# Kernel optimization log

Measured on AMD Instinct MI355X. Metric: run time of the kernel, lower is better.

Reference implementation:

```python
import jax, jax.numpy as jnp
import numpy as np

B, S, D = 8, 1024, 1024
H = 16
DK = D // H  # 64, dim_k == dim_v
F = 4096
EPS = 1e-5


def _layernorm(x, w, b):
    mu = jnp.mean(x, axis=-1, keepdims=True)
    var = jnp.mean((x - mu) ** 2, axis=-1, keepdims=True)
    return (x - mu) * jax.lax.rsqrt(var + EPS) * w + b


def setup_inputs() -> dict:
    key = jax.random.key(0)
    ks = jax.random.split(key, 12)
    init = lambda k, shape: (jax.random.normal(k, shape, dtype=jnp.float32) * 0.02)
    return {
        "src": jax.random.normal(ks[0], (B, S, D), dtype=jnp.float32),
        "mask": jnp.zeros((S, S), dtype=jnp.float32),
        # per-head projections, stacked over heads: [H, D, DK]
        "Wq": init(ks[1], (H, D, DK)), "bq": jnp.zeros((H, DK), jnp.float32),
        "Wk": init(ks[2], (H, D, DK)), "bk": jnp.zeros((H, DK), jnp.float32),
        "Wv": init(ks[3], (H, D, DK)), "bv": jnp.zeros((H, DK), jnp.float32),
        "Wo": init(ks[4], (H * DK, D)), "bo": jnp.zeros((D,), jnp.float32),
        "ln1_w": jnp.ones((D,), jnp.float32), "ln1_b": jnp.zeros((D,), jnp.float32),
        "W1": init(ks[5], (D, F)), "b1": jnp.zeros((F,), jnp.float32),
        "W2": init(ks[6], (F, D)), "b2": jnp.zeros((D,), jnp.float32),
        "ln2_w": jnp.ones((D,), jnp.float32), "ln2_b": jnp.zeros((D,), jnp.float32),
    }


def reference(src, mask, Wq, bq, Wk, bk, Wv, bv, Wo, bo,
              ln1_w, ln1_b, W1, b1, W2, b2, ln2_w, ln2_b):
    # per-head projections (vectorized over heads): [B, H, S, DK]
    q = jnp.einsum('bsd,hdk->bhsk', src, Wq) + bq[None, :, None, :]
    k = jnp.einsum('bsd,hdk->bhsk', src, Wk) + bk[None, :, None, :]
    v = jnp.einsum('bsd,hdk->bhsk', src, Wv) + bv[None, :, None, :]
    scale = float(DK) ** 0.5
    logits = jnp.einsum('bhsk,bhtk->bhst', q, k) / scale  # [B,H,S,S]
    logits = logits + mask * (-1e9)
    attn = jax.nn.softmax(logits, axis=-1)
    ctx = jnp.einsum('bhst,bhtv->bhsv', attn, v)  # [B,H,S,DK]
    # concat heads along feature dim (head-major order matches torch cat)
    ctx = jnp.transpose(ctx, (0, 2, 1, 3)).reshape(B, S, H * DK)
    attn_out = ctx @ Wo + bo
    x = _layernorm(src + attn_out, ln1_w, ln1_b)
    ffn = jax.nn.relu(x @ W1 + b1) @ W2 + b2
    return _layernorm(x + ffn, ln2_w, ln2_b)
```

## Files before the change

### kernel.cpp

```cpp
#include <hip/hip_runtime.h>

#define BB 8
#define SS 1024
#define DD 1024
#define HH 16
#define DK 64
#define FF 4096
#define MM (BB*SS)

typedef __attribute__((ext_vector_type(8))) short short8;
typedef __attribute__((ext_vector_type(4))) short short4v;
typedef __attribute__((ext_vector_type(4))) float floatx4;

__device__ inline short f2bf(float f) {
  union { float f; unsigned u; } v; v.f = f;
  unsigned r = (v.u + 0x7FFFu + ((v.u >> 16) & 1u)) >> 16;
  return (short)r;
}
__device__ inline float bf2f(unsigned short u) {
  union { unsigned u; float f; } v; v.u = ((unsigned)u) << 16;
  return v.f;
}

__device__ inline void gload_lds16(const void* g, void* l) {
  __builtin_amdgcn_global_load_lds(
      (const __attribute__((address_space(1))) void*)g,
      (__attribute__((address_space(3))) void*)l, 16, 0, 0);
}

__device__ void tr64(const float* __restrict__ s, unsigned short* __restrict__ d,
                     int R, int C, int r0, int c0, float (*ld)[68], int tid) {
  {
    int r = tid >> 2, c16 = (tid & 3) * 16;
#pragma unroll
    for (int i = 0; i < 4; ++i)
      *(float4*)(&ld[r][c16 + i * 4]) =
          *(const float4*)(s + (size_t)(r0 + r) * C + c0 + c16 + i * 4);
  }
  __syncthreads();
  int c = tid >> 2, r16 = (tid & 3) * 16;
  short8 o0, o1;
#pragma unroll
  for (int i = 0; i < 8; ++i) {
    o0[i] = f2bf(ld[r16 + i][c]);
    o1[i] = f2bf(ld[r16 + 8 + i][c]);
  }
  unsigned short* dp = d + (size_t)(c0 + c) * R + r0 + r16;
  *(short8*)(dp) = o0;
  *(short8*)(dp + 8) = o1;
}

__global__ __launch_bounds__(256) void prep_all(
    const float* __restrict__ src,
    const float* __restrict__ Wq, const float* __restrict__ Wk,
    const float* __restrict__ Wv,
    const float* __restrict__ bq, const float* __restrict__ bk,
    const float* __restrict__ bv, const float* __restrict__ Wo,
    unsigned short* __restrict__ srcb, unsigned short* __restrict__ wqkvT,
    float* __restrict__ bqkv, unsigned short* __restrict__ woT) {
  __shared__ float ld[64][68];
  const int bid = blockIdx.x, tid = threadIdx.x;
  if (bid < 4096) {
    int i8 = (bid * 256 + tid) * 8;
    float4 a = *(const float4*)(src + i8);
    float4 b = *(const float4*)(src + i8 + 4);
    short8 o;
    o[0] = f2bf(a.x); o[1] = f2bf(a.y); o[2] = f2bf(a.z); o[3] = f2bf(a.w);
    o[4] = f2bf(b.x); o[5] = f2bf(b.y); o[6] = f2bf(b.z); o[7] = f2bf(b.w);
    *(short8*)(srcb + i8) = o;
  } else if (bid < 4864) {
    int idx = bid - 4096;
    int d0 = (idx & 15) * 64, h = (idx >> 4) & 15, z = idx >> 8;
    const float* W = (z == 0 ? Wq : z == 1 ? Wk : Wv) + (size_t)h * DD * DK;
    {
      int r = tid >> 2, c16 = (tid & 3) * 16;
#pragma unroll
      for (int i = 0; i < 4; ++i)
        *(float4*)(&ld[r][c16 + i * 4]) =
            *(const float4*)(W + (size_t)(d0 + r) * DK + c16 + i * 4);
    }
    __syncthreads();
    int dv = tid >> 2, d16 = (tid & 3) * 16;
    short8 o0, o1;
#pragma unroll
    for (int i = 0; i < 8; ++i) {
      o0[i] = f2bf(ld[d16 + i][dv]);
      o1[i] = f2bf(ld[d16 + 8 + i][dv]);
    }
    unsigned short* dst = wqkvT + (size_t)(z * 1024 + h * 64 + dv) * DD + d0 + d16;
    *(short8*)(dst) = o0;
    *(short8*)(dst + 8) = o1;
  } else if (bid < 4876) {
    int n = (bid - 4864) * 256 + tid;
    int z = n >> 10;
    const float* s = (z == 0 ? bq : z == 1 ? bk : bv);
    bqkv[n] = s[n & 1023];
  } else {
    int idx = bid - 4876;
    tr64(Wo, woT, 1024, 1024, (idx & 15) * 64, (idx >> 4) * 64, ld, tid);
  }
}

__global__ __launch_bounds__(256) void prep2(
    const unsigned short* __restrict__ qkv, const float* __restrict__ mask,
    const float* __restrict__ W1, const float* __restrict__ W2,
    unsigned short* __restrict__ kbb, unsigned short* __restrict__ vtb,
    unsigned short* __restrict__ maskb, unsigned short* __restrict__ w1T,
    unsigned short* __restrict__ w2T) {
  __shared__ float ldf[64][68];
  const int bid = blockIdx.x, tid = threadIdx.x;
  if (bid < 2048) {
    const int t0 = (bid & 15) * 64, h = (bid >> 4) & 15, b = bid >> 8;
    int row = tid >> 2, c = (tid & 3) * 16;
    const unsigned short* s = qkv + (size_t)(b * SS + t0 + row) * 3072 + 1024 + h * 64 + c;
    unsigned short* d = kbb + ((size_t)((b * HH + h) * SS + t0 + row)) * 64 + c;
    *(short8*)(d) = *(const short8*)(s);
    *(short8*)(d + 8) = *(const short8*)(s + 8);
  } else if (bid < 4096) {
    __shared__ unsigned short ld[64][72];
    const int i = bid - 2048;
    const int t0 = (i & 15) * 64, h = (i >> 4) & 15, b = i >> 8;
    {
      int r = tid >> 2, c16 = (tid & 3) * 16;
      const unsigned short* s = qkv + (size_t)(b * SS + t0 + r) * 3072 + 2048 + h * 64 + c16;
      *(short8*)(&ld[r][c16]) = *(const short8*)(s);
      *(short8*)(&ld[r][c16 + 8]) = *(const short8*)(s + 8);
    }
    __syncthreads();
    int dv = tid >> 2, t16 = (tid & 3) * 16;
    short8 o0, o1;
#pragma unroll
    for (int j = 0; j < 8; ++j) {
      o0[j] = (short)ld[t16 + j][dv];
      o1[j] = (short)ld[t16 + 8 + j][dv];
    }
    unsigned short* d = vtb + ((size_t)(b * HH + h) * DK + dv) * SS + t0 + t16;
    *(short8*)(d) = o0;
    *(short8*)(d + 8) = o1;
  } else if (bid < 4608) {
    int i8 = ((bid - 4096) * 256 + tid) * 8;
    float4 a = *(const float4*)(mask + i8);
    float4 b = *(const float4*)(mask + i8 + 4);
    short8 o;
    o[0] = f2bf(a.x * -1e9f); o[1] = f2bf(a.y * -1e9f);
    o[2] = f2bf(a.z * -1e9f); o[3] = f2bf(a.w * -1e9f);
    o[4] = f2bf(b.x * -1e9f); o[5] = f2bf(b.y * -1e9f);
    o[6] = f2bf(b.z * -1e9f); o[7] = f2bf(b.w * -1e9f);
    *(short8*)(maskb + i8) = o;
  } else if (bid < 5632) {
    int i = bid - 4608;
    tr64(W1, w1T, 1024, 4096, (i & 15) * 64, (i >> 4) * 64, ldf, tid);
  } else {
    int i = bid - 5632;
    tr64(W2, w2T, 4096, 1024, (i & 63) * 64, (i >> 6) * 64, ldf, tid);
  }
}

#define BARE __builtin_amdgcn_s_barrier()
#define VM6  asm volatile("s_waitcnt vmcnt(6)" ::: "memory")
#define VM4  asm volatile("s_waitcnt vmcnt(4)" ::: "memory")
#define VM0  asm volatile("s_waitcnt vmcnt(0)" ::: "memory")
#define PH_HINT asm volatile("s_waitcnt lgkmcnt(8)" ::: "memory")
#define PH_SYNC { \
  __builtin_amdgcn_s_barrier(); \
  asm volatile("s_waitcnt lgkmcnt(0)" ::: "memory"); \
  __builtin_amdgcn_sched_barrier(0); }

#define LOAD_A(lA_, mh_) { \
  _Pragma("unroll") for (int m_ = 0; m_ < 4; ++m_) { \
    const int row_ = wr * 128 + (mh_) * 64 + m_ * 16 + lm; \
    _Pragma("unroll") for (int ks_ = 0; ks_ < 2; ++ks_) \
      a[m_][ks_] = *(const short8*)((lA_) + (size_t)row_ * 64 + \
                     (size_t)(((ks_ * 4 + quad) ^ (lm & 7)) * 8)); \
  } }

#define LOAD_B(lB_, nh_) { \
  _Pragma("unroll") for (int n_ = 0; n_ < 2; ++n_) { \
    const int row_ = wc * 64 + (nh_) * 32 + n_ * 16 + lm; \
    _Pragma("unroll") for (int ks_ = 0; ks_ < 2; ++ks_) \
      bfr[nh_][n_][ks_] = *(const short8*)((lB_) + 16384 + (size_t)row_ * 64 + \
                     (size_t)(((ks_ * 4 + quad) ^ (lm & 7)) * 8)); \
  } }

#define STAGE_A(kt_, mh_, lb_) { \
  _Pragma("unroll") for (int c_ = 0; c_ < 2; ++c_) { \
    const int row_ = c_ * 128 + (mh_) * 64; \
    gload_lds16(gA + (size_t)(kt_) * 64 + (size_t)row_ * K, \
                (lb_) + (size_t)(row_ + wave * 8) * 64); \
  } }

#define STAGE_B(kt_, nh_, lb_) { \
  _Pragma("unroll") for (int c_ = 0; c_ < 2; ++c_) { \
    const int row_ = c_ * 128 + hi128 + (nh_) * 32; \
    gload_lds16(gB + (size_t)(kt_) * 64 + (size_t)row_ * K, \
                (lb_) + 16384 + (size_t)(row_ + (wave & 3) * 8) * 64); \
  } }

#define MFMA_PH(mh_, nh_) { \
  __builtin_amdgcn_s_setprio(1); \
  _Pragma("unroll") for (int m_ = 0; m_ < 4; ++m_) \
    _Pragma("unroll") for (int n_ = 0; n_ < 2; ++n_) { \
      acc[(mh_) * 4 + m_][(nh_) * 2 + n_] = __builtin_amdgcn_mfma_f32_16x16x32_bf16( \
          bfr[nh_][n_][0], a[m_][0], acc[(mh_) * 4 + m_][(nh_) * 2 + n_], 0, 0, 0); \
      acc[(mh_) * 4 + m_][(nh_) * 2 + n_] = __builtin_amdgcn_mfma_f32_16x16x32_bf16( \
          bfr[nh_][n_][1], a[m_][1], acc[(mh_) * 4 + m_][(nh_) * 2 + n_], 0, 0, 0); \
    } \
  __builtin_amdgcn_s_setprio(0); }

#define KITER(e_, ST_) { \
  LOAD_A(buf0, 0); LOAD_B(buf0, 0); \
  STAGE_B((e_) + 1, 1, buf1); \
  PH_HINT; PH_SYNC; MFMA_PH(0, 0); BARE; \
  LOAD_B(buf0, 1); \
  if (ST_) STAGE_A((e_) + 2, 0, buf0); \
  PH_SYNC; MFMA_PH(0, 1); BARE; \
  LOAD_A(buf0, 1); \
  if (ST_) STAGE_B((e_) + 2, 0, buf0); \
  PH_SYNC; MFMA_PH(1, 0); BARE; \
  if (ST_) STAGE_A((e_) + 2, 1, buf0); \
  PH_SYNC; MFMA_PH(1, 1); \
  if (ST_) { VM6; } else { VM0; } \
  BARE; \
  LOAD_A(buf1, 0); LOAD_B(buf1, 0); \
  if (ST_) STAGE_B((e_) + 2, 1, buf0); \
  PH_HINT; PH_SYNC; MFMA_PH(0, 0); BARE; \
  LOAD_B(buf1, 1); \
  if (ST_) STAGE_A((e_) + 3, 0, buf1); \
  PH_SYNC; MFMA_PH(0, 1); BARE; \
  LOAD_A(buf1, 1); \
  if (ST_) STAGE_B((e_) + 3, 0, buf1); \
  PH_SYNC; MFMA_PH(1, 0); BARE; \
  if (ST_) { \
    STAGE_A((e_) + 3, 1, buf1); \
    PH_SYNC; MFMA_PH(1, 1); VM6; BARE; \
  } else { \
    PH_SYNC; MFMA_PH(1, 1); \
  } }

template <int RELU>
__global__ __launch_bounds__(512, 2) void gemm256(
    const unsigned short* __restrict__ A, const unsigned short* __restrict__ Bt,
    const float* __restrict__ bias, unsigned short* __restrict__ C,
    int M, int N, int K) {
  extern __shared__ unsigned short lds[];
  unsigned short* buf0 = lds;
  unsigned short* buf1 = lds + 32768;
  const int tid = threadIdx.x;
  const int wave = tid >> 6, lane = tid & 63;
  const int lm = lane & 15, quad = lane >> 4;
  const int wr = wave >> 2, wc = wave & 3;

  const int nwg = gridDim.x;
  const int cpx = nwg >> 3;
  const int id = (blockIdx.x & 7) * cpx + (blockIdx.x >> 3);
  const int nbx = N >> 8;
  const int bx = id % nbx, by = id / nbx;
  const int n0 = bx << 8, m0 = by << 8;

  const int NT = K >> 6;

  const int srow = tid >> 3;
  const int chs = (tid & 7) ^ (srow & 7);
  const int hi128 = (tid >= 256) ? 64 : 0;
  const int r32 = (tid >> 3) & 31;
  const unsigned short* gA = A + (size_t)(m0 + srow) * K + chs * 8;
  const unsigned short* gB = Bt + (size_t)(n0 + r32) * K + chs * 8;

  floatx4 acc[8][4] = {};
  short8 a[4][2], bfr[2][2][2];

  STAGE_A(0, 0, buf0); STAGE_B(0, 0, buf0);
  STAGE_A(0, 1, buf0); STAGE_B(0, 1, buf0);
  STAGE_A(1, 0, buf1); STAGE_B(1, 0, buf1);
  STAGE_A(1, 1, buf1);
  VM6;
  BARE;

  const int TT = NT >> 1;
  for (int i = 0; i < TT - 1; ++i) {
    KITER(2 * i, 1);
  }
  KITER(NT - 2, 0);

#pragma unroll
  for (int mi = 0; mi < 8; ++mi) {
    const int row = m0 + wr * 128 + mi * 16 + lm;
#pragma unroll
    for (int nj = 0; nj < 4; ++nj) {
      const int col = n0 + wc * 64 + nj * 16 + (quad << 2);
      const float4 bv = *(const float4*)(bias + col);
      float vv[4] = {acc[mi][nj][0] + bv.x, acc[mi][nj][1] + bv.y,
                     acc[mi][nj][2] + bv.z, acc[mi][nj][3] + bv.w};
      short4v o;
#pragma unroll
      for (int r = 0; r < 4; ++r) {
        float v = vv[r];
        if (RELU) v = fmaxf(v, 0.f);
        o[r] = f2bf(v);
      }
      *(short4v*)(C + (size_t)row * N + col) = o;
    }
  }
}

#define LOAD_A1(lb_, mh_) { \
  _Pragma("unroll") for (int m_ = 0; m_ < 2; ++m_) { \
    const int row_ = wr * 64 + (mh_) * 32 + m_ * 16 + lm; \
    _Pragma("unroll") for (int ks_ = 0; ks_ < 2; ++ks_) \
      a[m_][ks_] = *(const short8*)((lb_) + (size_t)row_ * 64 + \
                     (size_t)(((ks_ * 4 + quad) ^ (lm & 7)) * 8)); \
  } }

#define LOAD_B1(lb_, nh_) { \
  _Pragma("unroll") for (int n_ = 0; n_ < 2; ++n_) { \
    const int row_ = wc * 64 + (nh_) * 32 + n_ * 16 + lm; \
    _Pragma("unroll") for (int ks_ = 0; ks_ < 2; ++ks_) \
      bfr[nh_][n_][ks_] = *(const short8*)((lb_) + 8192 + (size_t)row_ * 64 + \
                     (size_t)(((ks_ * 4 + quad) ^ (lm & 7)) * 8)); \
  } }

#define STAGE_A1(kt_, mh_, lb_) { \
  gload_lds16(gA + (size_t)(kt_) * 64 + (size_t)((mh_) * 32) * K, \
              (lb_) + (size_t)((mh_) * 32 + hi128 + (wave & 3) * 8) * 64); }

#define STAGE_B1(kt_, nh_, lb_) { \
  _Pragma("unroll") for (int c_ = 0; c_ < 2; ++c_) { \
    const int row_ = c_ * 128 + hi128 + (nh_) * 32; \
    gload_lds16(gB + (size_t)(kt_) * 64 + (size_t)row_ * K, \
                (lb_) + 8192 + (size_t)(row_ + (wave & 3) * 8) * 64); \
  } }

#define MFMA_PH1(mh_, nh_) { \
  __builtin_amdgcn_s_setprio(1); \
  _Pragma("unroll") for (int m_ = 0; m_ < 2; ++m_) \
    _Pragma("unroll") for (int n_ = 0; n_ < 2; ++n_) { \
      acc[(mh_) * 2 + m_][(nh_) * 2 + n_] = __builtin_amdgcn_mfma_f32_16x16x32_bf16( \
          bfr[nh_][n_][0], a[m_][0], acc[(mh_) * 2 + m_][(nh_) * 2 + n_], 0, 0, 0); \
      acc[(mh_) * 2 + m_][(nh_) * 2 + n_] = __builtin_amdgcn_mfma_f32_16x16x32_bf16( \
          bfr[nh_][n_][1], a[m_][1], acc[(mh_) * 2 + m_][(nh_) * 2 + n_], 0, 0, 0); \
    } \
  __builtin_amdgcn_s_setprio(0); }

#define KITER1(e_, ST_) { \
  LOAD_A1(buf0, 0); LOAD_B1(buf0, 0); \
  STAGE_B1((e_) + 1, 1, buf1); \
  PH_SYNC; MFMA_PH1(0, 0); BARE; \
  LOAD_B1(buf0, 1); \
  if (ST_) STAGE_A1((e_) + 2, 0, buf0); \
  PH_SYNC; MFMA_PH1(0, 1); BARE; \
  LOAD_A1(buf0, 1); \
  if (ST_) STAGE_B1((e_) + 2, 0, buf0); \
  PH_SYNC; MFMA_PH1(1, 0); BARE; \
  if (ST_) STAGE_A1((e_) + 2, 1, buf0); \
  PH_SYNC; MFMA_PH1(1, 1); \
  if (ST_) { VM4; } else { VM0; } \
  BARE; \
  LOAD_A1(buf1, 0); LOAD_B1(buf1, 0); \
  if (ST_) STAGE_B1((e_) + 2, 1, buf0); \
  PH_SYNC; MFMA_PH1(0, 0); BARE; \
  LOAD_B1(buf1, 1); \
  if (ST_) STAGE_A1((e_) + 3, 0, buf1); \
  PH_SYNC; MFMA_PH1(0, 1); BARE; \
  LOAD_A1(buf1, 1); \
  if (ST_) STAGE_B1((e_) + 3, 0, buf1); \
  PH_SYNC; MFMA_PH1(1, 0); BARE; \
  if (ST_) { \
    STAGE_A1((e_) + 3, 1, buf1); \
    PH_SYNC; MFMA_PH1(1, 1); VM4; BARE; \
  } else { \
    PH_SYNC; MFMA_PH1(1, 1); \
  } }

__global__ __launch_bounds__(512, 2) void gemm128(
    const unsigned short* __restrict__ A, const unsigned short* __restrict__ Bt,
    const float* __restrict__ bias, unsigned short* __restrict__ C,
    int M, int N, int K) {
  extern __shared__ unsigned short lds[];
  unsigned short* buf0 = lds;
  unsigned short* buf1 = lds + 24576;
  const int tid = threadIdx.x;
  const int wave = tid >> 6, lane = tid & 63;
  const int lm = lane & 15, quad = lane >> 4;
  const int wr = wave >> 2, wc = wave & 3;

  const int nwg = gridDim.x;
  const int cpx = nwg >> 3;
  const int id = (blockIdx.x & 7) * cpx + (blockIdx.x >> 3);
  const int nbx = N >> 8;
  const int bx = id % nbx, by = id / nbx;
  const int n0 = bx << 8, m0 = by << 7;

  const int NT = K >> 6;

  const int srow = tid >> 3;
  const int chs = (tid & 7) ^ (srow & 7);
  const int hi128 = (tid >= 256) ? 64 : 0;
  const int r32 = (tid >> 3) & 31;
  const unsigned short* gA = A + (size_t)(m0 + hi128 + r32) * K + chs * 8;
  const unsigned short* gB = Bt + (size_t)(n0 + r32) * K + chs * 8;

  floatx4 acc[4][4] = {};
  short8 a[2][2], bfr[2][2][2];

  STAGE_A1(0, 0, buf0); STAGE_B1(0, 0, buf0);
  STAGE_A1(0, 1, buf0); STAGE_B1(0, 1, buf0);
  STAGE_A1(1, 0, buf1); STAGE_B1(1, 0, buf1);
  STAGE_A1(1, 1, buf1);
  VM4;
  BARE;

  const int TT = NT >> 1;
  for (int i = 0; i < TT - 1; ++i) {
    KITER1(2 * i, 1);
  }
  KITER1(NT - 2, 0);

#pragma unroll
  for (int mi = 0; mi < 4; ++mi) {
    const int row = m0 + wr * 64 + mi * 16 + lm;
#pragma unroll
    for (int nj = 0; nj < 4; ++nj) {
      const int col = n0 + wc * 64 + nj * 16 + (quad << 2);
      const float4 bv = *(const float4*)(bias + col);
      short4v o;
      o[0] = f2bf(acc[mi][nj][0] + bv.x);
      o[1] = f2bf(acc[mi][nj][1] + bv.y);
      o[2] = f2bf(acc[mi][nj][2] + bv.z);
      o[3] = f2bf(acc[mi][nj][3] + bv.w);
      *(short4v*)(C + (size_t)row * N + col) = o;
    }
  }
}

__global__ __launch_bounds__(512) void attention_flash(
    const unsigned short* __restrict__ qkv, const unsigned short* __restrict__ kb,
    const unsigned short* __restrict__ vt, const unsigned short* __restrict__ maskb,
    unsigned short* __restrict__ ctx) {
  const int flat = blockIdx.x;
  const int bh = (flat & 7) + 8 * (flat >> 6);
  const int qt = (flat >> 3) & 7;
  const int b = bh >> 4, h = bh & 15;
  const int s0 = qt * 128;
  const int tid = threadIdx.x;
  const int wave = tid >> 6, lane = tid & 63;
  const int lm = lane & 15, quad = lane >> 4;

  __shared__ __align__(16) unsigned short Ks[64 * 64];
  __shared__ __align__(16) unsigned short Vs[64 * 64];
  __shared__ __align__(16) unsigned short Ms[128 * 64];
  __shared__ __align__(16) unsigned short Ps[8][16 * 72];

  const unsigned short* qp = qkv + (size_t)(b * SS + s0 + wave * 16 + lm) * 3072 + h * 64;
  const short8 qa0 = *(const short8*)(qp + quad * 8);
  const short8 qa1 = *(const short8*)(qp + quad * 8 + 32);

  const unsigned short* kbase = kb + (size_t)bh * SS * DK;
  const unsigned short* vbase = vt + (size_t)bh * DK * SS;
  const unsigned short* mbase = maskb + (size_t)s0 * SS;

  const int sr = lane >> 3, sj = lane & 7;
  float m_run = -3e38f, l_run = 0.f;
  floatx4 O[4] = {};

  for (int it = 0; it < 16; ++it) {
    const int t0 = it * 64;
    __syncthreads();
    {
      int r = wave * 8 + sr;
      gload_lds16(kbase + (size_t)(t0 + r) * 64 + (size_t)(sj ^ (r & 7)) * 8,
                  (char*)Ks + wave * 1024);
      gload_lds16(vbase + (size_t)r * SS + t0 + (size_t)(sj ^ (r & 7)) * 8,
                  (char*)Vs + wave * 1024);
      int q1 = wave * 8 + sr;
      gload_lds16(mbase + (size_t)q1 * SS + t0 + (size_t)(sj ^ (q1 & 7)) * 8,
                  (char*)Ms + wave * 1024);
      int q2 = 64 + wave * 8 + sr;
      gload_lds16(mbase + (size_t)q2 * SS + t0 + (size_t)(sj ^ (q2 & 7)) * 8,
                  (char*)Ms + 8192 + wave * 1024);
    }
    __syncthreads();

    float p[16];
    float mt = -3e38f;
    const int qr = wave * 16 + lm;
#pragma unroll
    for (int ts = 0; ts < 4; ++ts) {
      int r = ts * 16 + lm;
      short8 kf0 = *(const short8*)&Ks[(r * 8 + (quad ^ (r & 7))) * 8];
      short8 kf1 = *(const short8*)&Ks[(r * 8 + ((quad + 4) ^ (r & 7))) * 8];
      floatx4 c = {0.f, 0.f, 0.f, 0.f};
      c = __builtin_amdgcn_mfma_f32_16x16x32_bf16(kf0, qa0, c, 0, 0, 0);
      c = __builtin_amdgcn_mfma_f32_16x16x32_bf16(kf1, qa1, c, 0, 0, 0);
      int mj = (ts * 2 + (quad >> 1)) ^ (qr & 7);
      short4v mv = *(const short4v*)&Ms[(qr * 8 + mj) * 8 + (quad & 1) * 4];
#pragma unroll
      for (int r2 = 0; r2 < 4; ++r2) {
        float sv = c[r2] * 0.125f + bf2f((unsigned short)mv[r2]);
        p[ts * 4 + r2] = sv;
        mt = fmaxf(mt, sv);
      }
    }
    mt = fmaxf(mt, __shfl_xor(mt, 16));
    mt = fmaxf(mt, __shfl_xor(mt, 32));
    if (!__all(mt - m_run <= 8.f)) {
      float mnew = fmaxf(m_run, mt);
      float alpha = __expf(m_run - mnew);
#pragma unroll
      for (int d = 0; d < 4; ++d)
#pragma unroll
        for (int r2 = 0; r2 < 4; ++r2) O[d][r2] *= alpha;
      l_run *= alpha;
      m_run = mnew;
    }
    float psum = 0.f;
#pragma unroll
    for (int i = 0; i < 16; ++i) { p[i] = __expf(p[i] - m_run); psum += p[i]; }
    psum += __shfl_xor(psum, 16);
    psum += __shfl_xor(psum, 32);
    l_run += psum;

    unsigned short* pw = &Ps[wave][lm * 72];
#pragma unroll
    for (int ts = 0; ts < 4; ++ts) {
      unsigned plo, phi;
      asm("v_cvt_pk_bf16_f32 %0, %1, %2" : "=v"(plo) : "v"(p[ts * 4 + 0]), "v"(p[ts * 4 + 1]));
      asm("v_cvt_pk_bf16_f32 %0, %1, %2" : "=v"(phi) : "v"(p[ts * 4 + 2]), "v"(p[ts * 4 + 3]));
      uint2 pu; pu.x = plo; pu.y = phi;
      *(uint2*)(pw + ts * 16 + quad * 4) = pu;
    }

#pragma unroll
    for (int ks = 0; ks < 2; ++ks) {
      short8 pf = *(const short8*)(pw + ks * 32 + quad * 8);
#pragma unroll
      for (int d = 0; d < 4; ++d) {
        int dv = d * 16 + lm;
        short8 vf = *(const short8*)&Vs[(dv * 8 + ((ks * 4 + quad) ^ (dv & 7))) * 8];
        O[d] = __builtin_amdgcn_mfma_f32_16x16x32_bf16(vf, pf, O[d], 0, 0, 0);
      }
    }
  }

  const float inv = 1.f / l_run;
  unsigned short* cp = ctx + (size_t)(b * SS + s0 + wave * 16 + lm) * DD + h * 64;
#pragma unroll
  for (int d = 0; d < 4; ++d) {
    short4v o;
#pragma unroll
    for (int r2 = 0; r2 < 4; ++r2) o[r2] = f2bf(O[d][r2] * inv);
    *(short4v*)(cp + d * 16 + quad * 4) = o;
  }
}

template <int A_BF16, int OUT_BF16>
__global__ __launch_bounds__(256) void residual_ln(
    const void* __restrict__ a_, const unsigned short* __restrict__ rr,
    const float* __restrict__ w, const float* __restrict__ bias,
    void* __restrict__ out_) {
  const int row = blockIdx.x;
  const int t = threadIdx.x;
  float x[4];
  if (A_BF16) {
    short4v va = *(const short4v*)((const unsigned short*)a_ + (size_t)row * DD + t * 4);
#pragma unroll
    for (int i = 0; i < 4; ++i) x[i] = bf2f((unsigned short)va[i]);
  } else {
    float4 va = *(const float4*)((const float*)a_ + (size_t)row * DD + t * 4);
    x[0] = va.x; x[1] = va.y; x[2] = va.z; x[3] = va.w;
  }
  {
    short4v vr = *(const short4v*)(rr + (size_t)row * DD + t * 4);
#pragma unroll
    for (int i = 0; i < 4; ++i) x[i] += bf2f((unsigned short)vr[i]);
  }
  float s = 0.f, ss = 0.f;
#pragma unroll
  for (int i = 0; i < 4; ++i) { s += x[i]; ss += x[i] * x[i]; }
#pragma unroll
  for (int o = 32; o > 0; o >>= 1) {
    s  += __shfl_down(s, o);
    ss += __shfl_down(ss, o);
  }
  __shared__ float2 sred[4];
  int wid = t >> 6;
  if ((t & 63) == 0) sred[wid] = make_float2(s, ss);
  __syncthreads();
  float st = 0.f, sst = 0.f;
#pragma unroll
  for (int i = 0; i < 4; ++i) { st += sred[i].x; sst += sred[i].y; }
  float mu  = st * (1.f / 1024.f);
  float var = sst * (1.f / 1024.f) - mu * mu;
  float rsq = rsqrtf(var + 1e-5f);
  float4 vw = *(const float4*)(w + t * 4);
  float4 vb = *(const float4*)(bias + t * 4);
  float o[4];
  o[0] = (x[0] - mu) * rsq * vw.x + vb.x;
  o[1] = (x[1] - mu) * rsq * vw.y + vb.y;
  o[2] = (x[2] - mu) * rsq * vw.z + vb.z;
  o[3] = (x[3] - mu) * rsq * vw.w + vb.w;
  if (OUT_BF16) {
    short4v ov;
#pragma unroll
    for (int i = 0; i < 4; ++i) ov[i] = f2bf(o[i]);
    *(short4v*)((unsigned short*)out_ + (size_t)row * DD + t * 4) = ov;
  } else {
    float4 ov = {o[0], o[1], o[2], o[3]};
    *(float4*)((float*)out_ + (size_t)row * DD + t * 4) = ov;
  }
}

extern "C" void kernel_launch(void* const* d_in, const int* in_sizes, int n_in,
                              void* d_out, int out_size, void* d_ws, size_t ws_size,
                              hipStream_t stream) {
  const float* src  = (const float*)d_in[0];
  const float* mask = (const float*)d_in[1];
  const float* Wq = (const float*)d_in[2];  const float* bq = (const float*)d_in[3];
  const float* Wk = (const float*)d_in[4];  const float* bk = (const float*)d_in[5];
  const float* Wv = (const float*)d_in[6];  const float* bv = (const float*)d_in[7];
  const float* Wo = (const float*)d_in[8];  const float* bo = (const float*)d_in[9];
  const float* ln1w = (const float*)d_in[10]; const float* ln1b = (const float*)d_in[11];
  const float* W1 = (const float*)d_in[12]; const float* b1 = (const float*)d_in[13];
  const float* W2 = (const float*)d_in[14]; const float* b2 = (const float*)d_in[15];
  const float* ln2w = (const float*)d_in[16]; const float* ln2b = (const float*)d_in[17];
  float* out = (float*)d_out;

  const size_t NEED = 125841408;
  if (ws_size < NEED) return;

  char* ws = (char*)d_ws;
  unsigned short* qkv   = (unsigned short*)(ws);
  unsigned short* vtb   = (unsigned short*)(ws + 50331648);
  unsigned short* kbb   = (unsigned short*)(ws + 67108864);
  unsigned short* ctxb  = (unsigned short*)(ws + 83886080);
  unsigned short* srcb  = (unsigned short*)(ws + 100663296);
  unsigned short* w1T   = (unsigned short*)(ws + 100663296);
  unsigned short* w2T   = (unsigned short*)(ws + 109051904);
  unsigned short* wqkvT = (unsigned short*)(ws + 117440512);
  unsigned short* maskb = (unsigned short*)(ws + 117440512);
  unsigned short* woT   = (unsigned short*)(ws + 123731968);
  float*          bqkv  = (float*)(ws + 125829120);
  unsigned short* h1       = qkv;
  unsigned short* attn_out = kbb;
  unsigned short* xb       = ctxb;
  unsigned short* ffn      = kbb;

  static bool lds_init = false;
  if (!lds_init) {
    auto* k0 = gemm256<0>;
    auto* k1 = gemm256<1>;
    hipFuncSetAttribute((const void*)k0, hipFuncAttributeMaxDynamicSharedMemorySize, 131072);
    hipFuncSetAttribute((const void*)k1, hipFuncAttributeMaxDynamicSharedMemorySize, 131072);
    hipFuncSetAttribute((const void*)gemm128, hipFuncAttributeMaxDynamicSharedMemorySize, 98304);
    lds_init = true;
  }

  prep_all<<<5132, 256, 0, stream>>>(src, Wq, Wk, Wv, bq, bk, bv, Wo,
                                     srcb, wqkvT, bqkv, woT);
  gemm128<<<(3072 / 256) * (MM / 128), 512, 98304, stream>>>(srcb, wqkvT, bqkv, qkv, MM, 3072, DD);
  prep2<<<6656, 256, 0, stream>>>(qkv, mask, W1, W2, kbb, vtb, maskb, w1T, w2T);
  attention_flash<<<1024, 512, 0, stream>>>(qkv, kbb, vtb, maskb, ctxb);
  gemm128<<<(DD / 256) * (MM / 128), 512, 98304, stream>>>(ctxb, woT, bo, attn_out, MM, DD, DD);
  residual_ln<0, 1><<<MM, 256, 0, stream>>>(src, attn_out, ln1w, ln1b, xb);
  gemm256<1><<<(FF / 256) * (MM / 256), 512, 131072, stream>>>(xb, w1T, b1, h1, MM, FF, DD);
  gemm128<<<(DD / 256) * (MM / 128), 512, 98304, stream>>>(h1, w2T, b2, ffn, MM, DD, FF);
  residual_ln<1, 0><<<MM, 256, 0, stream>>>(xb, ffn, ln2w, ln2b, out);
}
```

Before: 509.8 us.

## Read K directly from QKV buffer and use exp2 softmax in attention

Drops the separate K repack pass in prep2, so attention loads K tiles straight from the strided QKV projection output. The softmax is rewritten in base 2: scale and mask are pre-multiplied by log2(e) so the native exp2 instruction replaces __expf, and the rescale threshold is adjusted to match. The row max is computed with a tree of fmax instead of a serial chain. Strided K reads (3072-element row stride) may coalesce less well than the contiguous repacked layout.

```diff
diff --git a/kernel.cpp b/kernel.cpp
--- a/kernel.cpp
+++ b/kernel.cpp
@@ -104,21 +104,13 @@
 __global__ __launch_bounds__(256) void prep2(
     const unsigned short* __restrict__ qkv, const float* __restrict__ mask,
     const float* __restrict__ W1, const float* __restrict__ W2,
-    unsigned short* __restrict__ kbb, unsigned short* __restrict__ vtb,
-    unsigned short* __restrict__ maskb, unsigned short* __restrict__ w1T,
-    unsigned short* __restrict__ w2T) {
+    unsigned short* __restrict__ vtb, unsigned short* __restrict__ maskb,
+    unsigned short* __restrict__ w1T, unsigned short* __restrict__ w2T) {
   __shared__ float ldf[64][68];
   const int bid = blockIdx.x, tid = threadIdx.x;
   if (bid < 2048) {
-    const int t0 = (bid & 15) * 64, h = (bid >> 4) & 15, b = bid >> 8;
-    int row = tid >> 2, c = (tid & 3) * 16;
-    const unsigned short* s = qkv + (size_t)(b * SS + t0 + row) * 3072 + 1024 + h * 64 + c;
-    unsigned short* d = kbb + ((size_t)((b * HH + h) * SS + t0 + row)) * 64 + c;
-    *(short8*)(d) = *(const short8*)(s);
-    *(short8*)(d + 8) = *(const short8*)(s + 8);
-  } else if (bid < 4096) {
     __shared__ unsigned short ld[64][72];
-    const int i = bid - 2048;
+    const int i = bid;
     const int t0 = (i & 15) * 64, h = (i >> 4) & 15, b = i >> 8;
     {
       int r = tid >> 2, c16 = (tid & 3) * 16;
@@ -137,21 +129,22 @@
     unsigned short* d = vtb + ((size_t)(b * HH + h) * DK + dv) * SS + t0 + t16;
     *(short8*)(d) = o0;
     *(short8*)(d + 8) = o1;
-  } else if (bid < 4608) {
-    int i8 = ((bid - 4096) * 256 + tid) * 8;
+  } else if (bid < 2560) {
+    const float MS = -1.442695041e9f;
+    int i8 = ((bid - 2048) * 256 + tid) * 8;
     float4 a = *(const float4*)(mask + i8);
     float4 b = *(const float4*)(mask + i8 + 4);
     short8 o;
-    o[0] = f2bf(a.x * -1e9f); o[1] = f2bf(a.y * -1e9f);
-    o[2] = f2bf(a.z * -1e9f); o[3] = f2bf(a.w * -1e9f);
-    o[4] = f2bf(b.x * -1e9f); o[5] = f2bf(b.y * -1e9f);
-    o[6] = f2bf(b.z * -1e9f); o[7] = f2bf(b.w * -1e9f);
+    o[0] = f2bf(a.x * MS); o[1] = f2bf(a.y * MS);
+    o[2] = f2bf(a.z * MS); o[3] = f2bf(a.w * MS);
+    o[4] = f2bf(b.x * MS); o[5] = f2bf(b.y * MS);
+    o[6] = f2bf(b.z * MS); o[7] = f2bf(b.w * MS);
     *(short8*)(maskb + i8) = o;
-  } else if (bid < 5632) {
-    int i = bid - 4608;
+  } else if (bid < 3584) {
+    int i = bid - 2560;
     tr64(W1, w1T, 1024, 4096, (i & 15) * 64, (i >> 4) * 64, ldf, tid);
   } else {
-    int i = bid - 5632;
+    int i = bid - 3584;
     tr64(W2, w2T, 4096, 1024, (i & 63) * 64, (i >> 6) * 64, ldf, tid);
   }
 }
@@ -433,9 +426,8 @@
 }
 
 __global__ __launch_bounds__(512) void attention_flash(
-    const unsigned short* __restrict__ qkv, const unsigned short* __restrict__ kb,
-    const unsigned short* __restrict__ vt, const unsigned short* __restrict__ maskb,
-    unsigned short* __restrict__ ctx) {
+    const unsigned short* __restrict__ qkv, const unsigned short* __restrict__ vt,
+    const unsigned short* __restrict__ maskb, unsigned short* __restrict__ ctx) {
   const int flat = blockIdx.x;
   const int bh = (flat & 7) + 8 * (flat >> 6);
   const int qt = (flat >> 3) & 7;
@@ -454,11 +446,13 @@
   const short8 qa0 = *(const short8*)(qp + quad * 8);
   const short8 qa1 = *(const short8*)(qp + quad * 8 + 32);
 
-  const unsigned short* kbase = kb + (size_t)bh * SS * DK;
+  const unsigned short* kbase = qkv + (size_t)b * SS * 3072 + 1024 + h * 64;
   const unsigned short* vbase = vt + (size_t)bh * DK * SS;
   const unsigned short* mbase = maskb + (size_t)s0 * SS;
 
   const int sr = lane >> 3, sj = lane & 7;
+  const int srr = wave * 8 + sr;
+  const unsigned short* ksrc = kbase + (size_t)srr * 3072 + (size_t)(sj ^ (srr & 7)) * 8;
   float m_run = -3e38f, l_run = 0.f;
   floatx4 O[4] = {};
 
@@ -466,10 +460,8 @@
     const int t0 = it * 64;
     __syncthreads();
     {
-      int r = wave * 8 + sr;
-      gload_lds16(kbase + (size_t)(t0 + r) * 64 + (size_t)(sj ^ (r & 7)) * 8,
-                  (char*)Ks + wave * 1024);
-      gload_lds16(vbase + (size_t)r * SS + t0 + (size_t)(sj ^ (r & 7)) * 8,
+      gload_lds16(ksrc + (size_t)t0 * 3072, (char*)Ks + wave * 1024);
+      gload_lds16(vbase + (size_t)srr * SS + t0 + (size_t)(sj ^ (srr & 7)) * 8,
                   (char*)Vs + wave * 1024);
       int q1 = wave * 8 + sr;
       gload_lds16(mbase + (size_t)q1 * SS + t0 + (size_t)(sj ^ (q1 & 7)) * 8,
@@ -481,7 +473,6 @@
     __syncthreads();
 
     float p[16];
-    float mt = -3e38f;
     const int qr = wave * 16 + lm;
 #pragma unroll
     for (int ts = 0; ts < 4; ++ts) {
@@ -495,16 +486,20 @@
       short4v mv = *(const short4v*)&Ms[(qr * 8 + mj) * 8 + (quad & 1) * 4];
 #pragma unroll
       for (int r2 = 0; r2 < 4; ++r2) {
-        float sv = c[r2] * 0.125f + bf2f((unsigned short)mv[r2]);
-        p[ts * 4 + r2] = sv;
-        mt = fmaxf(mt, sv);
+        p[ts * 4 + r2] = c[r2] * 0.18033688011112042f + bf2f((unsigned short)mv[r2]);
       }
     }
+    float m0a = fmaxf(fmaxf(p[0], p[1]), p[2]);
+    float m0b = fmaxf(fmaxf(p[3], p[4]), p[5]);
+    float m0c = fmaxf(fmaxf(p[6], p[7]), p[8]);
+    float m0d = fmaxf(fmaxf(p[9], p[10]), p[11]);
+    float m0e = fmaxf(fmaxf(p[12], p[13]), p[14]);
+    float mt = fmaxf(fmaxf(fmaxf(m0a, m0b), m0c), fmaxf(fmaxf(m0d, m0e), p[15]));
     mt = fmaxf(mt, __shfl_xor(mt, 16));
     mt = fmaxf(mt, __shfl_xor(mt, 32));
-    if (!__all(mt - m_run <= 8.f)) {
+    if (!__all(mt - m_run <= 11.541560327f)) {
       float mnew = fmaxf(m_run, mt);
-      float alpha = __expf(m_run - mnew);
+      float alpha = __builtin_amdgcn_exp2f(m_run - mnew);
 #pragma unroll
       for (int d = 0; d < 4; ++d)
 #pragma unroll
@@ -514,7 +509,10 @@
     }
     float psum = 0.f;
 #pragma unroll
-    for (int i = 0; i < 16; ++i) { p[i] = __expf(p[i] - m_run); psum += p[i]; }
+    for (int i = 0; i < 16; ++i) {
+      p[i] = __builtin_amdgcn_exp2f(p[i] - m_run);
+      psum += p[i];
+    }
     psum += __shfl_xor(psum, 16);
     psum += __shfl_xor(psum, 32);
     l_run += psum;
@@ -657,8 +655,8 @@
   prep_all<<<5132, 256, 0, stream>>>(src, Wq, Wk, Wv, bq, bk, bv, Wo,
                                      srcb, wqkvT, bqkv, woT);
   gemm128<<<(3072 / 256) * (MM / 128), 512, 98304, stream>>>(srcb, wqkvT, bqkv, qkv, MM, 3072, DD);
-  prep2<<<6656, 256, 0, stream>>>(qkv, mask, W1, W2, kbb, vtb, maskb, w1T, w2T);
-  attention_flash<<<1024, 512, 0, stream>>>(qkv, kbb, vtb, maskb, ctxb);
+  prep2<<<4608, 256, 0, stream>>>(qkv, mask, W1, W2, vtb, maskb, w1T, w2T);
+  attention_flash<<<1024, 512, 0, stream>>>(qkv, vtb, maskb, ctxb);
   gemm128<<<(DD / 256) * (MM / 128), 512, 98304, stream>>>(ctxb, woT, bo, attn_out, MM, DD, DD);
   residual_ln<0, 1><<<MM, 256, 0, stream>>>(src, attn_out, ln1w, ln1b, xb);
   gemm256<1><<<(FF / 256) * (MM / 256), 512, 131072, stream>>>(xb, w1T, b1, h1, MM, FF, DD);
```

After: 518.9 us. About the same (+1.8%).
